# Kernel tuning notes

Measured on AMD Instinct MI355X. Metric: run time of the kernel, lower is better.

## Reference

```python
import jax, jax.numpy as jnp
import numpy as np

N_NODES = 50000
N_EDGES = 200000
NODE_DIM = 160     # node feat dim (divisible by 5 per wrapper slicing)
EDGE_DIM = 64      # latent edge feat dim
RAW_EDGE_DIM = 8   # raw geometric edge attributes
HID = 256          # hidden dim of edge/node update MLPs
ENC_HID = 128      # hidden dim of EASP edge encoder
N_ITER = 3
ENC_IN = 2 * NODE_DIM + RAW_EDGE_DIM                 # 328
EDGE_IN = 2 * 2 * NODE_DIM + 2 * EDGE_DIM            # 768 (reattach -> factor 2)
MSG_IN = 2 * NODE_DIM + EDGE_DIM                     # 384 (reattach node + edge)


def _ln(x, g, b):
    mu = jnp.mean(x, axis=-1, keepdims=True)
    v = jnp.var(x, axis=-1, keepdims=True)
    return (x - mu) * jax.lax.rsqrt(v + 1e-5) * g + b


def setup_inputs() -> dict:
    key = jax.random.key(0)
    ks = jax.random.split(key, 24)

    def w(k, shape):
        return (jax.random.normal(k, shape, jnp.float32) / np.sqrt(shape[0])).astype(jnp.float32)

    return {
        'x': jax.random.normal(ks[0], (N_NODES, NODE_DIM), jnp.float32),
        'edge_attr': jax.random.normal(ks[1], (N_EDGES, RAW_EDGE_DIM), jnp.float32),
        # EASP edge encoder MLP
        'enc_W1': w(ks[2], (ENC_IN, ENC_HID)), 'enc_b1': jnp.zeros((ENC_HID,), jnp.float32),
        'enc_W2': w(ks[3], (ENC_HID, EDGE_DIM)), 'enc_b2': jnp.zeros((EDGE_DIM,), jnp.float32),
        # EdgeCNN edge update MLP
        'eW1': w(ks[4], (EDGE_IN, HID)), 'eb1': jnp.zeros((HID,), jnp.float32),
        'eW2': w(ks[5], (HID, EDGE_DIM)), 'eb2': jnp.zeros((EDGE_DIM,), jnp.float32),
        # AttentionNodeUpdateNet: per-edge message MLP + attention vector + node out
        'mW1': w(ks[6], (MSG_IN, HID)), 'mb1': jnp.zeros((HID,), jnp.float32),
        'att_v': w(ks[7], (HID,)),
        'nW1': w(ks[8], (HID, NODE_DIM)), 'nb1': jnp.zeros((NODE_DIM,), jnp.float32),
        # shared LayerNorms (ModuleList([layer]*n_iter) shares one layer)
        'ln_ng': jnp.ones((NODE_DIM,), jnp.float32), 'ln_nb': jnp.zeros((NODE_DIM,), jnp.float32),
        'ln_eg': jnp.ones((EDGE_DIM,), jnp.float32), 'ln_eb': jnp.zeros((EDGE_DIM,), jnp.float32),
        'edge_row': jax.random.randint(ks[9], (N_EDGES,), 0, N_NODES, jnp.int32),
        'edge_col': jax.random.randint(ks[10], (N_EDGES,), 0, N_NODES, jnp.int32),
    }


def reference(x, edge_attr, enc_W1, enc_b1, enc_W2, enc_b2, eW1, eb1, eW2, eb2,
              mW1, mb1, att_v, nW1, nb1, ln_ng, ln_nb, ln_eg, ln_eb,
              edge_row, edge_col):
    row, col = edge_row, edge_col
    # edge encoder: gather endpoints, encode raw edge attrs
    init_edge = jnp.concatenate([x[row], x[col], edge_attr], axis=1)  # [E, 328]
    init_edge = jnp.maximum(init_edge @ enc_W1 + enc_b1, 0.0) @ enc_W2 + enc_b2  # [E, 64]

    node_lat, edge_lat = x, init_edge
    for _ in range(N_ITER):
        nl = jnp.concatenate([x, node_lat], axis=1)            # reattach initial node feats [N, 320]
        el = jnp.concatenate([init_edge, edge_lat], axis=1)    # reattach initial edge feats [E, 128]
        # edge update: gather-concat-MLP
        e_in = jnp.concatenate([nl[row], nl[col], el], axis=1)  # [E, 768]
        new_edge = jnp.maximum(e_in @ eW1 + eb1, 0.0) @ eW2 + eb2  # [E, 64]
        # node update: per-edge message + segment-softmax attention + scatter agg
        msg = jnp.maximum(jnp.concatenate([nl[col], new_edge], axis=1) @ mW1 + mb1, 0.0)  # [E, 256]
        logit = jax.nn.leaky_relu(msg @ att_v, 0.2)             # [E]
        smax = jax.ops.segment_max(logit, row, num_segments=N_NODES)
        ex = jnp.exp(logit - smax[row])
        den = jax.ops.segment_sum(ex, row, num_segments=N_NODES)
        alpha = ex / (den[row] + 1e-16)
        agg = jax.ops.segment_sum(alpha[:, None] * msg, row, num_segments=N_NODES)  # [N, 256]
        new_node = agg @ nW1 + nb1                              # [N, 160]
        # residual skip + (shared) LayerNorm
        node_lat = _ln(x + new_node, ln_ng, ln_nb)
        edge_lat = _ln(init_edge + new_edge, ln_eg, ln_eb)
    return node_lat, edge_lat
```

## Files before the change

kernel.cpp:

```cpp
#include <hip/hip_runtime.h>
#include <stdint.h>

#define N_NODES 50000
#define N_EDGES 200000
#define SCAN_B 512

typedef __bf16 bf16_t;
typedef bf16_t bf16x8 __attribute__((ext_vector_type(8)));
typedef float f32x4 __attribute__((ext_vector_type(4)));

__device__ __forceinline__ float bf2f(ushort h) {
  union { unsigned int u; float f; } c; c.u = ((unsigned int)h) << 16; return c.f;
}
__device__ __forceinline__ ushort f2bf(float f) {
  union { float f; unsigned int u; } c; c.f = f;
  unsigned int r = (c.u >> 16) & 1u;
  c.u += 0x7fffu + r;
  return (ushort)(c.u >> 16);
}
__device__ __forceinline__ float wave_sum(float v) {
#pragma unroll
  for (int m = 32; m > 0; m >>= 1) v += __shfl_xor(v, m, 64);
  return v;
}

__global__ void detect_k(const ushort* x, unsigned int* flag) {
  int i = blockIdx.x * 256 + threadIdx.x;
  unsigned int cnt = 0;
  for (int j = i; j < 1000000; j += 64 * 256) {
    ushort v = x[j];
    if (((v & 0x7F80u) == 0x7F80u) && (v & 0x7Fu)) cnt++;
  }
  if (cnt) atomicAdd(flag, cnt);
}

__global__ void cvt_in_k(const void* src, ushort* dst, int n, const unsigned int* flag) {
  int i = blockIdx.x * 256 + threadIdx.x;
  if (i >= n) return;
  if (*flag >= 2) dst[i] = f2bf(((const float*)src)[i]);
  else            dst[i] = ((const ushort*)src)[i];
}

__global__ void cvt_eattr_k(const void* src, const int* perm, ushort* dst,
                            const unsigned int* flag) {
  int i = blockIdx.x * 256 + threadIdx.x;
  if (i >= N_EDGES * 8) return;
  int e = i >> 3, j = i & 7;
  size_t o = (size_t)perm[e] * 8 + j;
  if (*flag >= 2) dst[i] = f2bf(((const float*)src)[o]);
  else            dst[i] = ((const ushort*)src)[o];
}

__global__ void transpose2_k(const void* W, ushort* Bt, int k0, int Ksrc, int Kpad,
                             int Wstride, const unsigned int* flag) {
  int k = blockIdx.x * 256 + threadIdx.x;
  int n = blockIdx.y;
  if (k >= Kpad) return;
  ushort v = 0;
  if (k < Ksrc) {
    if (*flag >= 2) v = f2bf(((const float*)W)[(size_t)(k0 + k) * Wstride + n]);
    else            v = ((const ushort*)W)[(size_t)(k0 + k) * Wstride + n];
  }
  Bt[(size_t)n * Kpad + k] = v;
}

__global__ void hist_k(const int* row, int* deg) {
  int e = blockIdx.x * 256 + threadIdx.x;
  if (e < N_EDGES) atomicAdd(&deg[row[e]], 1);
}
__global__ void scan_blk_k(const int* deg, int* off, int* bsum, int n) {
  __shared__ int s[SCAN_B];
  int i = blockIdx.x * SCAN_B + threadIdx.x;
  int v = (i < n) ? deg[i] : 0;
  s[threadIdx.x] = v;
  __syncthreads();
  for (int o = 1; o < SCAN_B; o <<= 1) {
    int t = (threadIdx.x >= o) ? s[threadIdx.x - o] : 0;
    __syncthreads();
    s[threadIdx.x] += t;
    __syncthreads();
  }
  if (i < n) off[i] = s[threadIdx.x] - v;
  if (threadIdx.x == SCAN_B - 1) bsum[blockIdx.x] = s[SCAN_B - 1];
}
__global__ void scan_top_k(int* bsum, int nb) {
  __shared__ int s[128];
  int v = (threadIdx.x < nb) ? bsum[threadIdx.x] : 0;
  s[threadIdx.x] = v;
  __syncthreads();
  for (int o = 1; o < 128; o <<= 1) {
    int t = (threadIdx.x >= o) ? s[threadIdx.x - o] : 0;
    __syncthreads();
    s[threadIdx.x] += t;
    __syncthreads();
  }
  if (threadIdx.x < nb) bsum[threadIdx.x] = s[threadIdx.x] - v;
}
__global__ void scan_add_k(int* off, const int* bsum, int n) {
  int i = blockIdx.x * 256 + threadIdx.x;
  if (i < n) off[i] += bsum[i >> 9];
  if (i == 0) off[n] = N_EDGES;
}
__global__ void fill_k(const int* row, const int* off, int* cur, int* perm) {
  int e = blockIdx.x * 256 + threadIdx.x;
  if (e >= N_EDGES) return;
  int r = row[e];
  int p = off[r] + atomicAdd(&cur[r], 1);
  perm[p] = e;
}
__global__ void gather_rc_k(const int* row, const int* col, const int* perm,
                            int* rs, int* cs) {
  int e = blockIdx.x * 256 + threadIdx.x;
  if (e >= N_EDGES) return;
  int o = perm[e];
  rs[e] = row[o];
  cs[e] = col[o];
}

struct GemmP {
  const ushort* X;
  const ushort* L;
  const ushort* E2;
  const float*  Af;
  const int* row;
  const int* col;
  const ushort* Bt;
  const ushort* bias;
  const ushort* Cr;
  const ushort* Cc;
  long cst;
  ushort* outb;  long ob_stride;
  ushort* outb2; long ob2_stride;
  ushort* outS;  long oS_stride;
  int nsplit;
  float*  outf;  long of_stride;
  long e2s;
  int M, K, Nw;
};

template <int MODE>
__device__ __forceinline__ uint4 load_a8(const GemmP& p, int e, int kg) {
  if (MODE == 0) {
    return *(const uint4*)(p.E2 + (size_t)e * p.e2s + kg);
  } else if (MODE == 5) {
    if (kg < 160) return *(const uint4*)(p.X + (size_t)e * 160 + kg);
    return *(const uint4*)(p.L + (size_t)e * 160 + (kg - 160));
  } else if (MODE == 7) {
    if (kg < 160) return *(const uint4*)(p.X + (size_t)e * 160 + kg);
    uint4 z; z.x = z.y = z.z = z.w = 0u; return z;
  } else if (MODE == 8) {
    if (kg < 8) return *(const uint4*)(p.E2 + (size_t)e * 8);
    uint4 z; z.x = z.y = z.z = z.w = 0u; return z;
  } else {
    const float* s = p.Af + (size_t)e * p.K + kg;
    f32x4 f0 = *(const f32x4*)s;
    f32x4 f1 = *(const f32x4*)(s + 4);
    union { ushort r[8]; uint4 u; } o;
    o.r[0] = f2bf(f0[0]); o.r[1] = f2bf(f0[1]); o.r[2] = f2bf(f0[2]); o.r[3] = f2bf(f0[3]);
    o.r[4] = f2bf(f1[0]); o.r[5] = f2bf(f1[1]); o.r[6] = f2bf(f1[2]); o.r[7] = f2bf(f1[3]);
    return o.u;
  }
}

template <int MODE, int CI, bool RELU, int NT>
__global__ __launch_bounds__(256) void gemm_k(GemmP p) {
  constexpr int BR = NT / 2;
  constexpr int NTC = NT * 16;
  constexpr int CIP = NTC + 8;
  __shared__ __align__(16) ushort smem[9216 + 1152 * NT];
  ushort* Asm = smem;
  ushort* Bsm = smem + 9216;
  const int t = threadIdx.x;
  const int w = t >> 6;
  const int l = t & 63;
  const int m0 = blockIdx.x * 128;
  const int n0 = blockIdx.y * NTC;

  const int srow = t >> 1;
  const int sph = (t & 1) << 5;
  int e = m0 + srow;
  if (e >= p.M) e = p.M - 1;

  int bn_[BR], bk_[BR];
#pragma unroll
  for (int j = 0; j < BR; j++) {
    int cid = j * 256 + t;
    bn_[j] = cid >> 3;
    bk_[j] = (cid & 7) << 3;
  }

  const int mq = l & 15;
  const int qd = l >> 4;

  uint4 ar[4];
  uint4 br[BR];
  auto load_tile = [&](int k0) {
#pragma unroll
    for (int j = 0; j < 4; j++)
      ar[j] = load_a8<MODE>(p, e, k0 + sph + j * 8);
#pragma unroll
    for (int j = 0; j < BR; j++)
      br[j] = *(const uint4*)(p.Bt + (size_t)(n0 + bn_[j]) * p.K + k0 + bk_[j]);
  };

  load_tile(0);

  f32x4 acc[2][NT] = {};
  if (CI) {
    const int gph = (t & 1) * (NTC / 2);
#pragma unroll
    for (int rd = 0; rd < ((CI == 1) ? 2 : 1); rd++) {
      int node = (rd == 0) ? p.col[e] : p.row[e];
      const ushort* base = ((rd == 0) ? p.Cc : p.Cr) + (size_t)node * p.cst + n0 + gph;
#pragma unroll
      for (int j = 0; j < NTC / 16; j++)
        *(uint4*)&smem[srow * CIP + gph + j * 8] = *(const uint4*)(base + j * 8);
      __syncthreads();
#pragma unroll
      for (int mt = 0; mt < 2; mt++) {
#pragma unroll
        for (int i = 0; i < 4; i++) {
          int rl = w * 32 + mt * 16 + qd * 4 + i;
#pragma unroll
          for (int nt = 0; nt < NT; nt++)
            acc[mt][nt][i] += bf2f(smem[rl * CIP + nt * 16 + mq]);
        }
      }
      __syncthreads();
    }
  }

  const int kiters = p.K >> 6;
  for (int kt = 0; kt < kiters; kt++) {
    __syncthreads();
#pragma unroll
    for (int j = 0; j < 4; j++)
      *(uint4*)&Asm[srow * 72 + sph + j * 8] = ar[j];
#pragma unroll
    for (int j = 0; j < BR; j++)
      *(uint4*)&Bsm[bn_[j] * 72 + bk_[j]] = br[j];
    if (kt + 1 < kiters) load_tile((kt + 1) << 6);
    __syncthreads();
#pragma unroll
    for (int ph = 0; ph < 2; ph++) {
      uint4 ra0 = *(const uint4*)&Asm[(w * 32 + mq) * 72 + ph * 32 + qd * 8];
      uint4 ra1 = *(const uint4*)&Asm[(w * 32 + 16 + mq) * 72 + ph * 32 + qd * 8];
      bf16x8 af0 = __builtin_bit_cast(bf16x8, ra0);
      bf16x8 af1 = __builtin_bit_cast(bf16x8, ra1);
#pragma unroll
      for (int nt = 0; nt < NT; nt++) {
        uint4 rb = *(const uint4*)&Bsm[(nt * 16 + mq) * 72 + ph * 32 + qd * 8];
        bf16x8 bfv = __builtin_bit_cast(bf16x8, rb);
        acc[0][nt] = __builtin_amdgcn_mfma_f32_16x16x32_bf16(af0, bfv, acc[0][nt], 0, 0, 0);
        acc[1][nt] = __builtin_amdgcn_mfma_f32_16x16x32_bf16(af1, bfv, acc[1][nt], 0, 0, 0);
      }
    }
  }

  if (MODE == 4) {
#pragma unroll
    for (int mt = 0; mt < 2; mt++) {
#pragma unroll
      for (int nt = 0; nt < NT; nt++) {
        int c = n0 + nt * 16 + mq;
        float bv = bf2f(p.bias[c]);
#pragma unroll
        for (int i = 0; i < 4; i++) {
          int r = m0 + w * 32 + mt * 16 + qd * 4 + i;
          if (r >= p.M) continue;
          float v = acc[mt][nt][i] + bv;
          if (RELU) v = fmaxf(v, 0.0f);
          p.outf[(size_t)r * p.of_stride + c] = v;
        }
      }
    }
  } else {
    ushort* dst = p.outb;
    long dstr = p.ob_stride;
    int nb0 = n0;
    if (p.outS && n0 >= p.nsplit) { dst = p.outS; dstr = p.oS_stride; nb0 = n0 - p.nsplit; }
    __syncthreads();
    ushort* S = smem + w * (32 * CIP);
#pragma unroll
    for (int mt = 0; mt < 2; mt++) {
#pragma unroll
      for (int nt = 0; nt < NT; nt++) {
        float bv = bf2f(p.bias[n0 + nt * 16 + mq]);
#pragma unroll
        for (int i = 0; i < 4; i++) {
          float v = acc[mt][nt][i] + bv;
          if (RELU) v = fmaxf(v, 0.0f);
          S[(mt * 16 + qd * 4 + i) * CIP + nt * 16 + mq] = f2bf(v);
        }
      }
    }
    __syncthreads();
#pragma unroll
    for (int j = 0; j < NT; j++) {
      int flat = (j * 64 + l) * 8;
      int lr = flat / NTC, cc = flat % NTC;
      int r = m0 + w * 32 + lr;
      if (r < p.M) {
        uint4 v = *(const uint4*)&S[lr * CIP + cc];
        *(uint4*)(dst + (size_t)r * dstr + nb0 + cc) = v;
        if (p.outb2) *(uint4*)(p.outb2 + (size_t)r * p.ob2_stride + n0 + cc) = v;
      }
    }
  }
}

__global__ void copy_u4_k(const uint4* s, uint4* d, int n) {
  int i = blockIdx.x * 256 + threadIdx.x;
  if (i < n) d[i] = s[i];
}

__global__ void agg_csr_k(const ushort* msg, const ushort* att, const int* off,
                          float* agg) {
  int n = blockIdx.x * 4 + (threadIdx.x >> 6);
  int l = threadIdx.x & 63;
  if (n >= N_NODES) return;
  const int s0 = off[n], s1 = off[n + 1];
  ushort4 av = *(const ushort4*)(att + l * 4);
  const float a0 = bf2f(av.x), a1 = bf2f(av.y), a2 = bf2f(av.z), a3 = bf2f(av.w);
  float maxl = -1e30f;
  for (int j = s0; j < s1; j++) {
    ushort4 m = *(const ushort4*)(msg + (size_t)j * 256 + l * 4);
    float d = bf2f(m.x) * a0 + bf2f(m.y) * a1 + bf2f(m.z) * a2 + bf2f(m.w) * a3;
    d = wave_sum(d);
    float lg = (d > 0.0f) ? d : 0.2f * d;
    maxl = fmaxf(maxl, lg);
  }
  float den = 0.0f;
  f32x4 acc = {0.0f, 0.0f, 0.0f, 0.0f};
  for (int j = s0; j < s1; j++) {
    ushort4 m = *(const ushort4*)(msg + (size_t)j * 256 + l * 4);
    float m0 = bf2f(m.x), m1 = bf2f(m.y), m2 = bf2f(m.z), m3 = bf2f(m.w);
    float d = m0 * a0 + m1 * a1 + m2 * a2 + m3 * a3;
    d = wave_sum(d);
    float lg = (d > 0.0f) ? d : 0.2f * d;
    float ex = __expf(lg - maxl);
    den += ex;
    acc[0] += ex * m0; acc[1] += ex * m1; acc[2] += ex * m2; acc[3] += ex * m3;
  }
  float inv = 1.0f / (den + 1e-16f);
  f32x4 o = {acc[0] * inv, acc[1] * inv, acc[2] * inv, acc[3] * inv};
  *(f32x4*)(agg + (size_t)n * 256 + l * 4) = o;
}

__global__ void ln_node_k(const ushort* x, const float* nn, const ushort* g,
                          const ushort* b, ushort* nlat) {
  int n = blockIdx.x * 4 + (threadIdx.x >> 6);
  int l = threadIdx.x & 63;
  if (n >= N_NODES) return;
  size_t bx = (size_t)n * 160;
  float v0 = bf2f(x[bx + l]) + nn[bx + l];
  float v1 = bf2f(x[bx + 64 + l]) + nn[bx + 64 + l];
  float v2 = (l < 32) ? (bf2f(x[bx + 128 + l]) + nn[bx + 128 + l]) : 0.0f;
  float mu = wave_sum(v0 + v1 + v2) * (1.0f / 160.0f);
  float d0 = v0 - mu, d1 = v1 - mu;
  float d2 = (l < 32) ? (v2 - mu) : 0.0f;
  float var = wave_sum(d0 * d0 + d1 * d1 + d2 * d2) * (1.0f / 160.0f);
  float inv = rsqrtf(var + 1e-5f);
  nlat[bx + l]      = f2bf(d0 * inv * bf2f(g[l])      + bf2f(b[l]));
  nlat[bx + 64 + l] = f2bf(d1 * inv * bf2f(g[64 + l]) + bf2f(b[64 + l]));
  if (l < 32)
    nlat[bx + 128 + l] = f2bf(d2 * inv * bf2f(g[128 + l]) + bf2f(b[128 + l]));
}

__global__ void ln_edge_k(const ushort* g, const ushort* b, ushort* el) {
  int e = blockIdx.x * 4 + (threadIdx.x >> 6);
  int l = threadIdx.x & 63;
  if (e >= N_EDGES) return;
  float v = bf2f(el[(size_t)e * 128 + l]) + bf2f(el[(size_t)e * 128 + 64 + l]);
  float mu = wave_sum(v) * (1.0f / 64.0f);
  float d = v - mu;
  float var = wave_sum(d * d) * (1.0f / 64.0f);
  float inv = rsqrtf(var + 1e-5f);
  el[(size_t)e * 128 + 64 + l] = f2bf(d * inv * bf2f(g[l]) + bf2f(b[l]));
}

__global__ void out_node_k(const ushort* nlat, void* out, const unsigned int* flag) {
  int i = blockIdx.x * 256 + threadIdx.x;
  if (i >= N_NODES * 160) return;
  if (*flag >= 2) ((float*)out)[i] = bf2f(nlat[i]);
  else            ((ushort*)out)[i] = nlat[i];
}
__global__ void out_edge_k(const ushort* el, const int* perm, void* out,
                           const unsigned int* flag) {
  int i = blockIdx.x * 256 + threadIdx.x;
  if (i >= N_EDGES * 64) return;
  int e = i >> 6, c = i & 63;
  ushort v = el[(size_t)e * 128 + 64 + c];
  size_t o = (size_t)N_NODES * 160 + (size_t)perm[e] * 64 + c;
  if (*flag >= 2) ((float*)out)[o] = bf2f(v);
  else            ((ushort*)out)[o] = v;
}

extern "C" void kernel_launch(void* const* d_in, const int* in_sizes, int n_in,
                              void* d_out, int out_size, void* d_ws, size_t ws_size,
                              hipStream_t stream) {
  const void* x_r     = d_in[0];
  const void* eattr_r = d_in[1];
  const void* encW1   = d_in[2];
  const void* encb1_r = d_in[3];
  const void* encW2   = d_in[4];
  const void* encb2_r = d_in[5];
  const void* eW1     = d_in[6];
  const void* eb1_r   = d_in[7];
  const void* eW2     = d_in[8];
  const void* eb2_r   = d_in[9];
  const void* mW1     = d_in[10];
  const void* mb1_r   = d_in[11];
  const void* attv_r  = d_in[12];
  const void* nW1     = d_in[13];
  const void* nb1_r   = d_in[14];
  const void* lnng_r  = d_in[15];
  const void* lnnb_r  = d_in[16];
  const void* lneg_r  = d_in[17];
  const void* lneb_r  = d_in[18];
  const int* erow = (const int*)d_in[19];
  const int* ecol = (const int*)d_in[20];
  (void)in_sizes; (void)n_in;

  char* ws = (char*)d_ws;
  size_t off = 0;
  auto alloc = [&](size_t bytes) -> void* {
    void* p = ws + off;
    off = (off + bytes + 511) & ~(size_t)511;
    return p;
  };
  ushort* hm   = (ushort*)alloc((size_t)N_EDGES * 256 * 2);
  ushort* el   = (ushort*)alloc((size_t)N_EDGES * 128 * 2);
  float*  agg  = (float*)alloc((size_t)N_NODES * 256 * 4);
  ushort* xc   = (ushort*)alloc((size_t)N_NODES * 160 * 2);
  ushort* nlat = (ushort*)alloc((size_t)N_NODES * 160 * 2);
  ushort* Qc   = (ushort*)alloc((size_t)N_NODES * 256 * 2);
  int* degcur  = (int*)alloc((size_t)2 * N_NODES * 4);
  int* offcsr  = (int*)alloc((size_t)(N_NODES + 1) * 4);
  int* perm    = (int*)alloc((size_t)N_EDGES * 4);
  int* rs      = (int*)alloc((size_t)N_EDGES * 4);
  int* cs      = (int*)alloc((size_t)N_EDGES * 4);
  int* bsum    = (int*)alloc((size_t)128 * 4);
  ushort* BtPe = (ushort*)alloc((size_t)256 * 192 * 2);
  ushort* BtWenc = (ushort*)alloc((size_t)128 * 64 * 2);
  ushort* BtE2 = (ushort*)alloc((size_t)64 * 128 * 2);
  ushort* BtPQ = (ushort*)alloc((size_t)768 * 320 * 2);
  ushort* BtWe = (ushort*)alloc((size_t)256 * 128 * 2);
  ushort* Bte2 = (ushort*)alloc((size_t)64 * 256 * 2);
  ushort* BtWm = (ushort*)alloc((size_t)256 * 64 * 2);
  ushort* Btn1 = (ushort*)alloc((size_t)160 * 256 * 2);
  ushort* pool = (ushort*)alloc((size_t)4096 * 2);
  unsigned int* flag = (unsigned int*)alloc(64);
  ushort* msg = hm;
  float*  nnf = (float*)hm;
  ushort* eac  = (ushort*)agg;
  ushort* Penc = (ushort*)((char*)agg + (size_t)N_EDGES * 8 * 2);
  ushort* Prc  = (ushort*)agg;
  ushort* zb   = pool + 2048;

  ushort* encb1c = pool;        ushort* encb2c = pool + 128;
  ushort* eb1c   = pool + 192;  ushort* eb2c   = pool + 448;
  ushort* mb1c   = pool + 512;  ushort* attvc  = pool + 768;
  ushort* nb1c   = pool + 1024; ushort* lnngc  = pool + 1184;
  ushort* lnnbc  = pool + 1344; ushort* lnegc  = pool + 1504;
  ushort* lnebc  = pool + 1568;

  if (off > ws_size) {
    hipMemsetAsync(d_out, 0, (size_t)out_size * 2, stream);
    return;
  }

  hipMemsetAsync(flag, 0, 64, stream);
  hipMemsetAsync(pool, 0, 4096 * 2, stream);
  hipMemsetAsync(degcur, 0, (size_t)2 * N_NODES * 4, stream);

  detect_k<<<64, 256, 0, stream>>>((const ushort*)x_r, flag);

  {
    int* deg = degcur;
    int* cur = degcur + N_NODES;
    const int nb = (N_NODES + SCAN_B - 1) / SCAN_B;
    hist_k<<<(N_EDGES + 255) / 256, 256, 0, stream>>>(erow, deg);
    scan_blk_k<<<nb, SCAN_B, 0, stream>>>(deg, offcsr, bsum, N_NODES);
    scan_top_k<<<1, 128, 0, stream>>>(bsum, nb);
    scan_add_k<<<(N_NODES + 255) / 256, 256, 0, stream>>>(offcsr, bsum, N_NODES);
    fill_k<<<(N_EDGES + 255) / 256, 256, 0, stream>>>(erow, offcsr, cur, perm);
    gather_rc_k<<<(N_EDGES + 255) / 256, 256, 0, stream>>>(erow, ecol, perm, rs, cs);
  }

  cvt_in_k<<<(N_NODES * 160 + 255) / 256, 256, 0, stream>>>(x_r, xc, N_NODES * 160, flag);
  cvt_eattr_k<<<(N_EDGES * 8 + 255) / 256, 256, 0, stream>>>(eattr_r, perm, eac, flag);
  cvt_in_k<<<1, 256, 0, stream>>>(encb1_r, encb1c, 128, flag);
  cvt_in_k<<<1, 256, 0, stream>>>(encb2_r, encb2c, 64, flag);
  cvt_in_k<<<1, 256, 0, stream>>>(eb1_r, eb1c, 256, flag);
  cvt_in_k<<<1, 256, 0, stream>>>(eb2_r, eb2c, 64, flag);
  cvt_in_k<<<1, 256, 0, stream>>>(mb1_r, mb1c, 256, flag);
  cvt_in_k<<<1, 256, 0, stream>>>(attv_r, attvc, 256, flag);
  cvt_in_k<<<1, 256, 0, stream>>>(nb1_r, nb1c, 160, flag);
  cvt_in_k<<<1, 256, 0, stream>>>(lnng_r, lnngc, 160, flag);
  cvt_in_k<<<1, 256, 0, stream>>>(lnnb_r, lnnbc, 160, flag);
  cvt_in_k<<<1, 256, 0, stream>>>(lneg_r, lnegc, 64, flag);
  cvt_in_k<<<1, 256, 0, stream>>>(lneb_r, lnebc, 64, flag);

  transpose2_k<<<dim3(1, 128), 256, 0, stream>>>(encW1, BtPe,             0, 160, 192, 128, flag);
  transpose2_k<<<dim3(1, 128), 256, 0, stream>>>(encW1, BtPe + 128 * 192, 160, 160, 192, 128, flag);
  transpose2_k<<<dim3(1, 128), 256, 0, stream>>>(encW1, BtWenc,           320, 8, 64, 128, flag);
  transpose2_k<<<dim3(1, 64), 256, 0, stream>>>(encW2, BtE2, 0, 128, 128, 64, flag);
  transpose2_k<<<dim3(2, 256), 256, 0, stream>>>(eW1, BtPQ,             0, 320, 320, 256, flag);
  transpose2_k<<<dim3(2, 256), 256, 0, stream>>>(eW1, BtPQ + 256 * 320, 320, 320, 320, 256, flag);
  transpose2_k<<<dim3(2, 256), 256, 0, stream>>>(mW1, BtPQ + 512 * 320, 0, 320, 320, 256, flag);
  transpose2_k<<<dim3(1, 256), 256, 0, stream>>>(eW1, BtWe, 640, 128, 128, 256, flag);
  transpose2_k<<<dim3(1, 64), 256, 0, stream>>>(eW2, Bte2, 0, 256, 256, 64, flag);
  transpose2_k<<<dim3(1, 256), 256, 0, stream>>>(mW1, BtWm, 320, 64, 64, 256, flag);
  transpose2_k<<<dim3(1, 160), 256, 0, stream>>>(nW1, Btn1, 0, 256, 256, 160, flag);

  copy_u4_k<<<(N_NODES * 160 / 8 + 255) / 256, 256, 0, stream>>>(
      (const uint4*)xc, (uint4*)nlat, N_NODES * 160 / 8);

  const int gE = (N_EDGES + 127) / 128;
  const int gN = (N_NODES + 127) / 128;

  {
    GemmP p{};
    p.X = xc; p.Bt = BtPe; p.bias = zb;
    p.outb = Penc; p.ob_stride = 256;
    p.M = N_NODES; p.K = 192; p.Nw = 256;
    gemm_k<7, 0, false, 8><<<dim3(gN, 2), 256, 0, stream>>>(p);
  }
  {
    GemmP p{};
    p.E2 = eac; p.row = rs; p.col = cs;
    p.Cr = Penc; p.Cc = Penc + 128; p.cst = 256;
    p.Bt = BtWenc; p.bias = encb1c;
    p.outb = hm; p.ob_stride = 128;
    p.M = N_EDGES; p.K = 64; p.Nw = 128;
    gemm_k<8, 1, true, 8><<<dim3(gE, 1), 256, 0, stream>>>(p);
  }
  {
    GemmP p{};
    p.E2 = hm; p.e2s = 128; p.Bt = BtE2; p.bias = encb2c;
    p.outb = el; p.ob_stride = 128;
    p.outb2 = el + 64; p.ob2_stride = 128;
    p.M = N_EDGES; p.K = 128; p.Nw = 64;
    gemm_k<0, 0, false, 4><<<dim3(gE, 1), 256, 0, stream>>>(p);
  }

  for (int it = 0; it < 3; it++) {
    {
      GemmP p{};
      p.X = xc; p.L = nlat; p.Bt = BtPQ; p.bias = zb;
      p.outb = Prc; p.ob_stride = 512;
      p.outS = Qc; p.oS_stride = 256; p.nsplit = 512;
      p.M = N_NODES; p.K = 320; p.Nw = 768;
      gemm_k<5, 0, false, 8><<<dim3(gN, 6), 256, 0, stream>>>(p);
    }
    {
      GemmP p{};
      p.E2 = el; p.e2s = 128; p.row = rs; p.col = cs;
      p.Cr = Prc; p.Cc = Prc + 256; p.cst = 512;
      p.Bt = BtWe; p.bias = eb1c;
      p.outb = hm; p.ob_stride = 256;
      p.M = N_EDGES; p.K = 128; p.Nw = 256;
      gemm_k<0, 1, true, 8><<<dim3(gE, 2), 256, 0, stream>>>(p);
    }
    {
      GemmP p{};
      p.E2 = hm; p.e2s = 256; p.Bt = Bte2; p.bias = eb2c;
      p.outb = el + 64; p.ob_stride = 128;
      p.M = N_EDGES; p.K = 256; p.Nw = 64;
      gemm_k<0, 0, false, 4><<<dim3(gE, 1), 256, 0, stream>>>(p);
    }
    {
      GemmP p{};
      p.E2 = el + 64; p.e2s = 128; p.row = rs; p.col = cs;
      p.Cc = Qc; p.cst = 256;
      p.Bt = BtWm; p.bias = mb1c;
      p.outb = msg; p.ob_stride = 256;
      p.M = N_EDGES; p.K = 64; p.Nw = 256;
      gemm_k<0, 2, true, 8><<<dim3(gE, 2), 256, 0, stream>>>(p);
    }
    ln_edge_k<<<N_EDGES / 4, 256, 0, stream>>>(lnegc, lnebc, el);
    agg_csr_k<<<(N_NODES + 3) / 4, 256, 0, stream>>>(msg, attvc, offcsr, agg);
    {
      GemmP p{};
      p.Af = agg; p.Bt = Btn1; p.bias = nb1c;
      p.outf = nnf; p.of_stride = 160;
      p.M = N_NODES; p.K = 256; p.Nw = 160;
      gemm_k<4, 0, false, 10><<<dim3(gN, 1), 256, 0, stream>>>(p);
    }
    ln_node_k<<<(N_NODES + 3) / 4, 256, 0, stream>>>(xc, nnf, lnngc, lnnbc, nlat);
  }

  out_node_k<<<(N_NODES * 160 + 255) / 256, 256, 0, stream>>>(nlat, d_out, flag);
  out_edge_k<<<(N_EDGES * 64 + 255) / 256, 256, 0, stream>>>(el, perm, d_out, flag);
  (void)out_size;
}
```

Measured before the change: 1.875 ms.

## Fuse node residual+LayerNorm into output GEMM epilogue; per-wave gather staging

The node-output GEMM epilogue now adds the residual x and bias, computes the LayerNorm over the 160 columns with intra-row shuffles, and writes bf16 node latents directly. The separate ln_node_k kernel and its fp32 intermediate round-trip are removed. Separately, the gathered-node prologue in the edge GEMMs stages rows in per-wave shared-memory slices and replaces the block-wide barriers with lgkmcnt waits. This relies on each wave only reading the rows it wrote itself, and on the shuffle reduction covering exactly the lanes that share a row.

Result: slower. 1.918 ms (+2.3%).

```diff
diff --git a/kernel.cpp b/kernel.cpp
--- a/kernel.cpp
+++ b/kernel.cpp
@@ -162,7 +162,7 @@
   }
 }
 
-template <int MODE, int CI, bool RELU, int NT>
+template <int MODE, int CI, bool RELU, int NT, bool LNN>
 __global__ __launch_bounds__(256) void gemm_k(GemmP p) {
   constexpr int BR = NT / 2;
   constexpr int NTC = NT * 16;
@@ -207,26 +207,33 @@
 
   f32x4 acc[2][NT] = {};
   if (CI) {
-    const int gph = (t & 1) * (NTC / 2);
+    ushort* Wl = smem + w * (32 * CIP);
+    const int rr = l >> 1;
+    const int hf = (l & 1) * (NTC / 2);
+    int er = m0 + w * 32 + rr;
+    if (er >= p.M) er = p.M - 1;
+    const int nodec = p.col[er];
+    const int noder = (CI == 1) ? p.row[er] : 0;
 #pragma unroll
     for (int rd = 0; rd < ((CI == 1) ? 2 : 1); rd++) {
-      int node = (rd == 0) ? p.col[e] : p.row[e];
-      const ushort* base = ((rd == 0) ? p.Cc : p.Cr) + (size_t)node * p.cst + n0 + gph;
+      const ushort* base = ((rd == 0) ? p.Cc + (size_t)nodec * p.cst
+                                      : p.Cr + (size_t)noder * p.cst) + n0 + hf;
 #pragma unroll
       for (int j = 0; j < NTC / 16; j++)
-        *(uint4*)&smem[srow * CIP + gph + j * 8] = *(const uint4*)(base + j * 8);
-      __syncthreads();
+        *(uint4*)&Wl[rr * CIP + hf + j * 8] = *(const uint4*)(base + j * 8);
+      asm volatile("s_waitcnt lgkmcnt(0)" ::: "memory");
 #pragma unroll
       for (int mt = 0; mt < 2; mt++) {
 #pragma unroll
         for (int i = 0; i < 4; i++) {
-          int rl = w * 32 + mt * 16 + qd * 4 + i;
+          const int rl = mt * 16 + qd * 4 + i;
 #pragma unroll
           for (int nt = 0; nt < NT; nt++)
-            acc[mt][nt][i] += bf2f(smem[rl * CIP + nt * 16 + mq]);
+            acc[mt][nt][i] += bf2f(Wl[rl * CIP + nt * 16 + mq]);
         }
       }
-      __syncthreads();
+      if (CI == 1 && rd == 0)
+        asm volatile("s_waitcnt lgkmcnt(0)" ::: "memory");
     }
   }
 
@@ -258,19 +265,56 @@
   }
 
   if (MODE == 4) {
-#pragma unroll
-    for (int mt = 0; mt < 2; mt++) {
-#pragma unroll
-      for (int nt = 0; nt < NT; nt++) {
-        int c = n0 + nt * 16 + mq;
-        float bv = bf2f(p.bias[c]);
+    if (LNN) {
+#pragma unroll
+      for (int mt = 0; mt < 2; mt++) {
 #pragma unroll
         for (int i = 0; i < 4; i++) {
           int r = m0 + w * 32 + mt * 16 + qd * 4 + i;
-          if (r >= p.M) continue;
-          float v = acc[mt][nt][i] + bv;
-          if (RELU) v = fmaxf(v, 0.0f);
-          p.outf[(size_t)r * p.of_stride + c] = v;
+          int rc = (r < p.M) ? r : p.M - 1;
+          float vals[NT];
+          float s = 0.0f;
+#pragma unroll
+          for (int nt = 0; nt < NT; nt++) {
+            int c = n0 + nt * 16 + mq;
+            float v = acc[mt][nt][i] + bf2f(p.bias[c]) +
+                      bf2f(p.X[(size_t)rc * p.of_stride + c]);
+            vals[nt] = v; s += v;
+          }
+#pragma unroll
+          for (int m = 1; m <= 8; m <<= 1) s += __shfl_xor(s, m, 64);
+          float mu = s * (1.0f / 160.0f);
+          float ss = 0.0f;
+#pragma unroll
+          for (int nt = 0; nt < NT; nt++) { float d = vals[nt] - mu; ss += d * d; }
+#pragma unroll
+          for (int m = 1; m <= 8; m <<= 1) ss += __shfl_xor(ss, m, 64);
+          float inv = rsqrtf(ss * (1.0f / 160.0f) + 1e-5f);
+          if (r < p.M) {
+#pragma unroll
+            for (int nt = 0; nt < NT; nt++) {
+              int c = n0 + nt * 16 + mq;
+              float o = (vals[nt] - mu) * inv * bf2f(p.Cr[c]) + bf2f(p.Cc[c]);
+              p.outb[(size_t)r * p.ob_stride + c] = f2bf(o);
+            }
+          }
+        }
+      }
+    } else {
+#pragma unroll
+      for (int mt = 0; mt < 2; mt++) {
+#pragma unroll
+        for (int nt = 0; nt < NT; nt++) {
+          int c = n0 + nt * 16 + mq;
+          float bv = bf2f(p.bias[c]);
+#pragma unroll
+          for (int i = 0; i < 4; i++) {
+            int r = m0 + w * 32 + mt * 16 + qd * 4 + i;
+            if (r >= p.M) continue;
+            float v = acc[mt][nt][i] + bv;
+            if (RELU) v = fmaxf(v, 0.0f);
+            p.outf[(size_t)r * p.of_stride + c] = v;
+          }
         }
       }
     }
@@ -345,26 +389,6 @@
   float inv = 1.0f / (den + 1e-16f);
   f32x4 o = {acc[0] * inv, acc[1] * inv, acc[2] * inv, acc[3] * inv};
   *(f32x4*)(agg + (size_t)n * 256 + l * 4) = o;
-}
-
-__global__ void ln_node_k(const ushort* x, const float* nn, const ushort* g,
-                          const ushort* b, ushort* nlat) {
-  int n = blockIdx.x * 4 + (threadIdx.x >> 6);
-  int l = threadIdx.x & 63;
-  if (n >= N_NODES) return;
-  size_t bx = (size_t)n * 160;
-  float v0 = bf2f(x[bx + l]) + nn[bx + l];
-  float v1 = bf2f(x[bx + 64 + l]) + nn[bx + 64 + l];
-  float v2 = (l < 32) ? (bf2f(x[bx + 128 + l]) + nn[bx + 128 + l]) : 0.0f;
-  float mu = wave_sum(v0 + v1 + v2) * (1.0f / 160.0f);
-  float d0 = v0 - mu, d1 = v1 - mu;
-  float d2 = (l < 32) ? (v2 - mu) : 0.0f;
-  float var = wave_sum(d0 * d0 + d1 * d1 + d2 * d2) * (1.0f / 160.0f);
-  float inv = rsqrtf(var + 1e-5f);
-  nlat[bx + l]      = f2bf(d0 * inv * bf2f(g[l])      + bf2f(b[l]));
-  nlat[bx + 64 + l] = f2bf(d1 * inv * bf2f(g[64 + l]) + bf2f(b[64 + l]));
-  if (l < 32)
-    nlat[bx + 128 + l] = f2bf(d2 * inv * bf2f(g[128 + l]) + bf2f(b[128 + l]));
 }
 
 __global__ void ln_edge_k(const ushort* g, const ushort* b, ushort* el) {
@@ -452,7 +476,6 @@
   ushort* pool = (ushort*)alloc((size_t)4096 * 2);
   unsigned int* flag = (unsigned int*)alloc(64);
   ushort* msg = hm;
-  float*  nnf = (float*)hm;
   ushort* eac  = (ushort*)agg;
   ushort* Penc = (ushort*)((char*)agg + (size_t)N_EDGES * 8 * 2);
   ushort* Prc  = (ushort*)agg;
@@ -525,7 +548,7 @@
     p.X = xc; p.Bt = BtPe; p.bias = zb;
     p.outb = Penc; p.ob_stride = 256;
     p.M = N_NODES; p.K = 192; p.Nw = 256;
-    gemm_k<7, 0, false, 8><<<dim3(gN, 2), 256, 0, stream>>>(p);
+    gemm_k<7, 0, false, 8, false><<<dim3(gN, 2), 256, 0, stream>>>(p);
   }
   {
     GemmP p{};
@@ -534,7 +557,7 @@
     p.Bt = BtWenc; p.bias = encb1c;
     p.outb = hm; p.ob_stride = 128;
     p.M = N_EDGES; p.K = 64; p.Nw = 128;
-    gemm_k<8, 1, true, 8><<<dim3(gE, 1), 256, 0, stream>>>(p);
+    gemm_k<8, 1, true, 8, false><<<dim3(gE, 1), 256, 0, stream>>>(p);
   }
   {
     GemmP p{};
@@ -542,7 +565,7 @@
     p.outb = el; p.ob_stride = 128;
     p.outb2 = el + 64; p.ob2_stride = 128;
     p.M = N_EDGES; p.K = 128; p.Nw = 64;
-    gemm_k<0, 0, false, 4><<<dim3(gE, 1), 256, 0, stream>>>(p);
+    gemm_k<0, 0, false, 4, false><<<dim3(gE, 1), 256, 0, stream>>>(p);
   }
 
   for (int it = 0; it < 3; it++) {
@@ -552,7 +575,7 @@
       p.outb = Prc; p.ob_stride = 512;
       p.outS = Qc; p.oS_stride = 256; p.nsplit = 512;
       p.M = N_NODES; p.K = 320; p.Nw = 768;
-      gemm_k<5, 0, false, 8><<<dim3(gN, 6), 256, 0, stream>>>(p);
+      gemm_k<5, 0, false, 8, false><<<dim3(gN, 6), 256, 0, stream>>>(p);
     }
     {
       GemmP p{};
@@ -561,14 +584,14 @@
       p.Bt = BtWe; p.bias = eb1c;
       p.outb = hm; p.ob_stride = 256;
       p.M = N_EDGES; p.K = 128; p.Nw = 256;
-      gemm_k<0, 1, true, 8><<<dim3(gE, 2), 256, 0, stream>>>(p);
+      gemm_k<0, 1, true, 8, false><<<dim3(gE, 2), 256, 0, stream>>>(p);
     }
     {
       GemmP p{};
       p.E2 = hm; p.e2s = 256; p.Bt = Bte2; p.bias = eb2c;
       p.outb = el + 64; p.ob_stride = 128;
       p.M = N_EDGES; p.K = 256; p.Nw = 64;
-      gemm_k<0, 0, false, 4><<<dim3(gE, 1), 256, 0, stream>>>(p);
+      gemm_k<0, 0, false, 4, false><<<dim3(gE, 1), 256, 0, stream>>>(p);
     }
     {
       GemmP p{};
@@ -577,18 +600,19 @@
       p.Bt = BtWm; p.bias = mb1c;
       p.outb = msg; p.ob_stride = 256;
       p.M = N_EDGES; p.K = 64; p.Nw = 256;
-      gemm_k<0, 2, true, 8><<<dim3(gE, 2), 256, 0, stream>>>(p);
+      gemm_k<0, 2, true, 8, false><<<dim3(gE, 2), 256, 0, stream>>>(p);
     }
     ln_edge_k<<<N_EDGES / 4, 256, 0, stream>>>(lnegc, lnebc, el);
     agg_csr_k<<<(N_NODES + 3) / 4, 256, 0, stream>>>(msg, attvc, offcsr, agg);
     {
       GemmP p{};
       p.Af = agg; p.Bt = Btn1; p.bias = nb1c;
-      p.outf = nnf; p.of_stride = 160;
+      p.X = xc; p.of_stride = 160;
+      p.Cr = lnngc; p.Cc = lnnbc;
+      p.outb = nlat; p.ob_stride = 160;
       p.M = N_NODES; p.K = 256; p.Nw = 160;
-      gemm_k<4, 0, false, 10><<<dim3(gN, 1), 256, 0, stream>>>(p);
-    }
-    ln_node_k<<<(N_NODES + 3) / 4, 256, 0, stream>>>(xc, nnf, lnngc, lnnbc, nlat);
+      gemm_k<4, 0, false, 10, true><<<dim3(gN, 1), 256, 0, stream>>>(p);
+    }
   }
 
   out_node_k<<<(N_NODES * 160 + 255) / 256, 256, 0, stream>>>(nlat, d_out, flag);
```
